# Kernel tuning notes

Hardware: AMD Instinct MI355X
Metric: run time of the kernel (lower is better)

The kernel has to match this reference:

```python
import jax, jax.numpy as jnp
import numpy as np

BITS = 4
GROUP = 128
IN_F = 4096
OUT_F = 11008
N_GROUPS = IN_F // GROUP  # padded_in == in_features here


def fwht(v):
    """Orthonormal fast Walsh-Hadamard transform over the last axis (len = power of 2)."""
    orig = v.shape
    g = orig[-1]
    x = v.reshape(-1, g)
    h = 1
    while h < g:
        x = x.reshape(-1, g // (2 * h), 2, h)
        a, b = x[:, :, 0, :], x[:, :, 1, :]
        x = jnp.stack([a + b, a - b], axis=2).reshape(-1, g)
        h *= 2
    return (x * (1.0 / np.sqrt(g))).reshape(orig)


def setup_inputs() -> dict:
    key = jax.random.key(0)
    ks = jax.random.split(key, 7)
    x = jax.random.normal(ks[0], (4096, IN_F), dtype=jnp.float32)
    # packed 4-bit indices: two per byte, stored as int32 byte values
    packed_weight = jax.random.randint(ks[1], (OUT_F, IN_F // 2), 0, 256, dtype=jnp.int32)
    # per-(row, group) scale factors (positive)
    norms = jax.random.uniform(ks[2], (OUT_F, N_GROUPS), dtype=jnp.float32) * 0.1 + 0.01
    # Lloyd-Max codebook: 2^bits sorted centroids
    centroids = jnp.sort(jax.random.normal(ks[3], (2 ** BITS,), dtype=jnp.float32))
    # Rademacher sign vectors for the two-round signed WHT rotation
    signs1 = jnp.where(jax.random.normal(ks[4], (GROUP,)) >= 0, 1.0, -1.0).astype(jnp.float32)
    signs2 = jnp.where(jax.random.normal(ks[5], (GROUP,)) >= 0, 1.0, -1.0).astype(jnp.float32)
    bias = jax.random.normal(ks[6], (OUT_F,), dtype=jnp.float32) * 0.01
    return {"x": x, "packed_weight": packed_weight, "norms": norms,
            "centroids": centroids, "signs1": signs1, "signs2": signs2, "bias": bias}


def dequantize(packed_weight, norms, centroids, signs1, signs2):
    out_f, n_groups = norms.shape
    # unpack 4-bit nibbles: low nibble at even positions, high nibble at odd
    pw = packed_weight.astype(jnp.uint8)
    lo = (pw & 15).astype(jnp.int32)
    hi = (pw >> 4).astype(jnp.int32)
    idx = jnp.stack([lo, hi], axis=-1).reshape(out_f, -1)      # [out, padded_in]
    c = centroids[idx].reshape(out_f, n_groups, GROUP)          # codebook lookup
    # inverse of rotate(v) = H(s2 * H(s1 * v)):  v = s1 * H(s2 * H(u))
    u = fwht(c) * signs2
    u = fwht(u) * signs1
    w = u * norms[:, :, None]                                   # per-group rescale
    return w.reshape(out_f, -1)


def reference(x, packed_weight, norms, centroids, signs1, signs2, bias):
    w = dequantize(packed_weight, norms, centroids, signs1, signs2)[:, : x.shape[-1]]
    return x @ w.T + bias
```

## Files before the change

kernel.cpp:

```cpp
#include <hip/hip_runtime.h>
#include <stdint.h>

#define M_DIM 4096
#define K_DIM 4096
#define N_DIM 11008
#define N_GROUPS 32

typedef __attribute__((ext_vector_type(8))) short short8;
typedef __attribute__((ext_vector_type(4))) float floatx4;

__device__ __forceinline__ unsigned short f32_to_bf16(float f) {
    unsigned int u = __float_as_uint(f);
    unsigned int rounding = 0x7FFFu + ((u >> 16) & 1u);
    return (unsigned short)((u + rounding) >> 16);
}

__global__ __launch_bounds__(128) void make_M_kernel(
    const float* __restrict__ signs1, const float* __restrict__ signs2,
    unsigned short* __restrict__ Mt)
{
    const int i = blockIdx.x;
    const int j = threadIdx.x;
    __shared__ float s2s[128];
    s2s[j] = signs2[j];
    __syncthreads();
    float acc = 0.f;
#pragma unroll 8
    for (int a = 0; a < 128; ++a) {
        int par = (__popc(i & a) + __popc(a & j)) & 1;
        acc += par ? -s2s[a] : s2s[a];
    }
    Mt[i * 128 + j] = f32_to_bf16(signs1[j] * acc * (1.0f / 128.0f));
}

#define TX_RS 136

__global__ __launch_bounds__(256) void transform_x_kernel(
    const float* __restrict__ x,
    const unsigned short* __restrict__ Mt,
    unsigned short* __restrict__ z)
{
    __shared__ __align__(16) short Xs[64 * TX_RS];
    __shared__ __align__(16) short Ms[128 * TX_RS];

    const int tid = threadIdx.x;
    const int wave = tid >> 6, lane = tid & 63;
    const int col16 = lane & 15, quad = lane >> 4;
    const int m0 = (blockIdx.x >> 5) * 64;
    const int g = blockIdx.x & 31;
    const int c0 = g * 128;

#pragma unroll
    for (int it = 0; it < 8; ++it) {
        int idx = tid + 256 * it;
        int row = idx >> 5, c4 = idx & 31;
        float4 v = *(const float4*)(x + (size_t)(m0 + row) * K_DIM + c0 + c4 * 4);
        uint2 o;
        o.x = (unsigned)f32_to_bf16(v.x) | ((unsigned)f32_to_bf16(v.y) << 16);
        o.y = (unsigned)f32_to_bf16(v.z) | ((unsigned)f32_to_bf16(v.w) << 16);
        *(uint2*)(Xs + row * TX_RS + c4 * 4) = o;
    }
#pragma unroll
    for (int it = 0; it < 8; ++it) {
        int ch = tid + 256 * it;
        int row = ch >> 4, cc = ch & 15;
        uint4 v = *(const uint4*)(Mt + (size_t)ch * 8);
        *(uint4*)(Ms + row * TX_RS + cc * 8) = v;
    }
    __syncthreads();

    floatx4 acc[8] = {};
#pragma unroll
    for (int ks = 0; ks < 4; ++ks) {
        short8 af = *(const short8*)(Xs + (wave * 16 + col16) * TX_RS + ks * 32 + quad * 8);
#pragma unroll
        for (int ni = 0; ni < 8; ++ni) {
            short8 bf = *(const short8*)(Ms + (ni * 16 + col16) * TX_RS + ks * 32 + quad * 8);
            acc[ni] = __builtin_amdgcn_mfma_f32_16x16x32_bf16(af, bf, acc[ni], 0, 0, 0);
        }
    }
#pragma unroll
    for (int ni = 0; ni < 8; ++ni)
#pragma unroll
        for (int r = 0; r < 4; ++r) {
            int row = m0 + wave * 16 + quad * 4 + r;
            z[(size_t)row * K_DIM + c0 + ni * 16 + col16] = f32_to_bf16(acc[ni][r]);
        }
}

__global__ __launch_bounds__(256) void dequant_lut_kernel(
    const int* __restrict__ packed,
    const float* __restrict__ norms,
    const float* __restrict__ centroids,
    unsigned int* __restrict__ w_out)
{
    __shared__ float2 lut[256];
    const int tid = threadIdx.x;
    lut[tid] = make_float2(centroids[tid & 15], centroids[tid >> 4]);
    __syncthreads();

    const int row = blockIdx.x;
    const int g = tid >> 3;
    const float nrm = norms[row * N_GROUPS + g];
    const int* prow = packed + (size_t)row * 2048 + tid * 8;
    int4 pa = *(const int4*)(prow);
    int4 pb = *(const int4*)(prow + 4);
    int v[8] = {pa.x, pa.y, pa.z, pa.w, pb.x, pb.y, pb.z, pb.w};
    unsigned o[8];
#pragma unroll
    for (int q = 0; q < 8; ++q) {
        float2 c = lut[v[q] & 255];
        o[q] = (unsigned)f32_to_bf16(c.x * nrm) | ((unsigned)f32_to_bf16(c.y * nrm) << 16);
    }
    unsigned* orow = w_out + (size_t)row * 2048 + tid * 8;
    *(uint4*)(orow)     = make_uint4(o[0], o[1], o[2], o[3]);
    *(uint4*)(orow + 4) = make_uint4(o[4], o[5], o[6], o[7]);
}

#define BM 256
#define BN 256
#define BK 64

typedef const __attribute__((address_space(1))) void* gvp_t;
typedef __attribute__((address_space(3))) void* svp_t;

#define BARRIER() do { asm volatile("" ::: "memory"); __builtin_amdgcn_s_barrier(); \
                       asm volatile("" ::: "memory"); } while (0)
#define VM8()   asm volatile("s_waitcnt vmcnt(8)" ::: "memory")
#define VM4()   asm volatile("s_waitcnt vmcnt(4)" ::: "memory")
#define VM2()   asm volatile("s_waitcnt vmcnt(2)" ::: "memory")
#define VM0()   asm volatile("s_waitcnt vmcnt(0)" ::: "memory")
#define PRIO1() __builtin_amdgcn_s_setprio(1)
#define PRIO0() __builtin_amdgcn_s_setprio(0)

__device__ __forceinline__ void read_a4(short8 (&dst)[4][2], const short* rb, int s0) {
#pragma unroll
    for (int fm = 0; fm < 4; ++fm) {
        dst[fm][0] = *(const short8*)(rb + fm * 1024 + s0);
        dst[fm][1] = *(const short8*)(rb + fm * 1024 + (s0 ^ 32));
    }
}
__device__ __forceinline__ void read_b2(short8 (&dst)[2][2], const short* rb, int s0) {
#pragma unroll
    for (int fn = 0; fn < 2; ++fn) {
        dst[fn][0] = *(const short8*)(rb + fn * 1024 + s0);
        dst[fn][1] = *(const short8*)(rb + fn * 1024 + (s0 ^ 32));
    }
}
__device__ __forceinline__ void mfma_q(floatx4 (&acc)[4][2],
                                       const short8 (&a)[4][2], const short8 (&b)[2][2]) {
#pragma unroll
    for (int ks = 0; ks < 2; ++ks)
#pragma unroll
        for (int fm = 0; fm < 4; ++fm)
#pragma unroll
            for (int fn = 0; fn < 2; ++fn)
                acc[fm][fn] = __builtin_amdgcn_mfma_f32_16x16x32_bf16(
                    a[fm][ks], b[fn][ks], acc[fm][fn], 0, 0, 0);
}

__global__ __launch_bounds__(512, 2) void gemm_bt_kernel(
    const unsigned short* __restrict__ A,
    const unsigned short* __restrict__ B,
    const float* __restrict__ bias,
    float* __restrict__ C)
{
    __shared__ __align__(16) short smem[65536];
    short* As = smem;
    short* Bs = smem + 32768;

    const int tid = threadIdx.x;
    const int w = tid >> 6, lane = tid & 63;
    const int wm = w >> 2, wn = w & 3;
    const int col16 = lane & 15, quad = lane >> 4;

    const int bid = blockIdx.x;
    const int mt = bid & 15;
    const int nt = bid >> 4;
    const int m0 = mt * BM, n0 = nt * BN;

    const int gc = (lane & 7) ^ (lane >> 3);
    const unsigned short* aSrc = A + (size_t)(m0 + w * 8 + (lane >> 3)) * K_DIM + gc * 8;
    const unsigned short* bSrc = B + (size_t)(n0 + (w >> 2) * 64 + (w & 3) * 8 + (lane >> 3)) * K_DIM + gc * 8;
    const int wOff = w * 512;

#define STAGE_A(BUF, H, KT) do { \
    __builtin_amdgcn_global_load_lds((gvp_t)(aSrc + (size_t)((H) * 64) * K_DIM + (KT) * 64), \
        (svp_t)(As + (BUF) * 16384 + (H) * 8192 + wOff), 16, 0, 0); \
    __builtin_amdgcn_global_load_lds((gvp_t)(aSrc + (size_t)((H) * 64 + 128) * K_DIM + (KT) * 64), \
        (svp_t)(As + (BUF) * 16384 + (H) * 8192 + 4096 + wOff), 16, 0, 0); \
} while (0)
#define STAGE_B(BUF, H, KT) do { \
    __builtin_amdgcn_global_load_lds((gvp_t)(bSrc + (size_t)((H) * 32) * K_DIM + (KT) * 64), \
        (svp_t)(Bs + (BUF) * 16384 + (H) * 8192 + wOff), 16, 0, 0); \
    __builtin_amdgcn_global_load_lds((gvp_t)(bSrc + (size_t)((H) * 32 + 128) * K_DIM + (KT) * 64), \
        (svp_t)(Bs + (BUF) * 16384 + (H) * 8192 + 4096 + wOff), 16, 0, 0); \
} while (0)

    const short* aR = As + (wm * 64 + col16) * 64;
    const short* bR = Bs + (wn * 32 + col16) * 64;
    const int s0 = (quad ^ (col16 & 7)) << 3;

    short8 a0[4][2], a1[4][2], b0[2][2], b1[2][2];
    floatx4 acc[2][2][4][2];
#pragma unroll
    for (int i0 = 0; i0 < 2; ++i0)
#pragma unroll
        for (int i1 = 0; i1 < 2; ++i1)
#pragma unroll
            for (int i2 = 0; i2 < 4; ++i2)
#pragma unroll
                for (int i3 = 0; i3 < 2; ++i3)
                    acc[i0][i1][i2][i3] = (floatx4)0.0f;


    STAGE_A(0, 0, 0); STAGE_B(0, 0, 0);
    STAGE_A(0, 1, 0); STAGE_B(0, 1, 0);
    STAGE_A(1, 0, 1); STAGE_B(1, 0, 1);
    VM8();
    BARRIER();
    read_a4(a0, aR, s0); read_b2(b0, bR, s0);
    STAGE_A(1, 1, 1);
    VM8();
    BARRIER();

    const int NIT = K_DIM / (2 * BK) - 1;
    for (int i = 0; i < NIT; ++i) {
        const int t = 2 * i;
        read_a4(a1, aR + 8192, s0);
        PRIO1(); mfma_q(acc[0][0], a0, b0); PRIO0();
        STAGE_B(1, 1, t + 1);
        VM8(); BARRIER();
        read_b2(b1, bR + 8192, s0);
        PRIO1(); mfma_q(acc[1][0], a1, b0); PRIO0();
        STAGE_A(0, 0, t + 2);
        BARRIER();
        PRIO1(); mfma_q(acc[0][1], a0, b1); PRIO0();
        STAGE_B(0, 0, t + 2);
        VM8(); BARRIER();
        read_a4(a0, aR + 16384, s0); read_b2(b0, bR + 16384, s0);
        PRIO1(); mfma_q(acc[1][1], a1, b1); PRIO0();
        STAGE_A(0, 1, t + 2);
        VM8(); BARRIER();
        read_a4(a1, aR + 16384 + 8192, s0);
        PRIO1(); mfma_q(acc[0][0], a0, b0); PRIO0();
        STAGE_B(0, 1, t + 2);
        VM8(); BARRIER();
        read_b2(b1, bR + 16384 + 8192, s0);
        PRIO1(); mfma_q(acc[1][0], a1, b0); PRIO0();
        STAGE_A(1, 0, t + 3);
        BARRIER();
        PRIO1(); mfma_q(acc[0][1], a0, b1); PRIO0();
        STAGE_B(1, 0, t + 3);
        VM8(); BARRIER();
        read_a4(a0, aR, s0); read_b2(b0, bR, s0);
        PRIO1(); mfma_q(acc[1][1], a1, b1); PRIO0();
        STAGE_A(1, 1, t + 3);
        VM8(); BARRIER();
    }

    read_a4(a1, aR + 8192, s0);
    mfma_q(acc[0][0], a0, b0);
    STAGE_B(1, 1, 63);
    VM8();
    BARRIER();
    read_b2(b1, bR + 8192, s0);
    mfma_q(acc[1][0], a1, b0);
    VM4();
    BARRIER();
    mfma_q(acc[0][1], a0, b1);
    VM2();
    BARRIER();
    read_a4(a0, aR + 16384, s0); read_b2(b0, bR + 16384, s0);
    mfma_q(acc[1][1], a1, b1);
    VM0();
    BARRIER();
    read_a4(a1, aR + 16384 + 8192, s0);
    mfma_q(acc[0][0], a0, b0);
    read_b2(b1, bR + 16384 + 8192, s0);
    mfma_q(acc[1][0], a1, b0);
    mfma_q(acc[0][1], a0, b1);
    mfma_q(acc[1][1], a1, b1);

#undef STAGE_A
#undef STAGE_B

    float bv[2][2];
#pragma unroll
    for (int qn = 0; qn < 2; ++qn)
#pragma unroll
        for (int fn = 0; fn < 2; ++fn)
            bv[qn][fn] = bias[n0 + wn * 64 + qn * 32 + fn * 16 + col16];

#pragma unroll
    for (int qm = 0; qm < 2; ++qm)
#pragma unroll
        for (int fm = 0; fm < 4; ++fm)
#pragma unroll
            for (int r = 0; r < 4; ++r) {
                float* crow = C + (size_t)(m0 + wm * 128 + qm * 64 + fm * 16 + quad * 4 + r) * N_DIM
                              + n0 + wn * 64 + col16;
#pragma unroll
                for (int qn = 0; qn < 2; ++qn)
#pragma unroll
                    for (int fn = 0; fn < 2; ++fn)
                        crow[qn * 32 + fn * 16] = acc[qm][qn][fm][fn][r] + bv[qn][fn];
            }
}

extern "C" void kernel_launch(void* const* d_in, const int* in_sizes, int n_in,
                              void* d_out, int out_size, void* d_ws, size_t ws_size,
                              hipStream_t stream) {
    const float* x        = (const float*)d_in[0];
    const int* packed     = (const int*)d_in[1];
    const float* norms    = (const float*)d_in[2];
    const float* centroids= (const float*)d_in[3];
    const float* signs1   = (const float*)d_in[4];
    const float* signs2   = (const float*)d_in[5];
    const float* bias     = (const float*)d_in[6];
    float* out            = (float*)d_out;

    unsigned short* Mt     = (unsigned short*)d_ws;
    unsigned short* w_bf16 = (unsigned short*)((char*)d_ws + 32768);
    unsigned short* z_bf16 = (unsigned short*)((char*)d_ws + 32768 + (size_t)N_DIM * K_DIM * 2);

    make_M_kernel<<<128, 128, 0, stream>>>(signs1, signs2, Mt);

    transform_x_kernel<<<(M_DIM / 64) * N_GROUPS, 256, 0, stream>>>(x, Mt, z_bf16);

    dequant_lut_kernel<<<N_DIM, 256, 0, stream>>>(
        packed, norms, centroids, (unsigned int*)w_bf16);

    gemm_bt_kernel<<<dim3((M_DIM / BM) * (N_DIM / BN)), 512, 0, stream>>>(
        z_bf16, w_bf16, bias, out);
}
```

Baseline: 593.8 us.

## Restructure x-transform with LDS-staged stores, bank-spread LUT, nontemporal output stores

The x-transform kernel now uses 512-thread blocks that each handle 256 rows in four 64-row steps. Each block keeps its Hadamard-matrix fragments in registers and stages results through LDS so the z writes are coalesced 16-byte stores. The dequant LUT becomes a per-lane replicated 16x32 table to avoid LDS bank conflicts, and the GEMM epilogue writes output with nontemporal stores to reduce cache pollution. The costs are more LDS, extra barriers, and a grid of fewer, larger blocks for the transform.

```diff
diff --git a/kernel.cpp b/kernel.cpp
--- a/kernel.cpp
+++ b/kernel.cpp
@@ -33,59 +33,88 @@
     Mt[i * 128 + j] = f32_to_bf16(signs1[j] * acc * (1.0f / 128.0f));
 }
 
-#define TX_RS 136
-
-__global__ __launch_bounds__(256) void transform_x_kernel(
+__global__ __launch_bounds__(512) void transform_x_kernel(
     const float* __restrict__ x,
     const unsigned short* __restrict__ Mt,
     unsigned short* __restrict__ z)
 {
-    __shared__ __align__(16) short Xs[64 * TX_RS];
-    __shared__ __align__(16) short Ms[128 * TX_RS];
+    __shared__ __align__(16) short Ms[128 * 136];
+    __shared__ __align__(16) short Xs[64 * 136];
+    __shared__ __align__(16) short Ls[64 * 136];
 
     const int tid = threadIdx.x;
     const int wave = tid >> 6, lane = tid & 63;
     const int col16 = lane & 15, quad = lane >> 4;
-    const int m0 = (blockIdx.x >> 5) * 64;
+    const int wr = wave >> 2;
+    const int wc = wave & 3;
     const int g = blockIdx.x & 31;
+    const int mblk = blockIdx.x >> 5;
     const int c0 = g * 128;
-
-#pragma unroll
-    for (int it = 0; it < 8; ++it) {
-        int idx = tid + 256 * it;
-        int row = idx >> 5, c4 = idx & 31;
-        float4 v = *(const float4*)(x + (size_t)(m0 + row) * K_DIM + c0 + c4 * 4);
-        uint2 o;
-        o.x = (unsigned)f32_to_bf16(v.x) | ((unsigned)f32_to_bf16(v.y) << 16);
-        o.y = (unsigned)f32_to_bf16(v.z) | ((unsigned)f32_to_bf16(v.w) << 16);
-        *(uint2*)(Xs + row * TX_RS + c4 * 4) = o;
-    }
-#pragma unroll
-    for (int it = 0; it < 8; ++it) {
-        int ch = tid + 256 * it;
+    const int mBase = mblk * 256;
+
+#pragma unroll
+    for (int it = 0; it < 4; ++it) {
+        int ch = tid + 512 * it;
         int row = ch >> 4, cc = ch & 15;
-        uint4 v = *(const uint4*)(Mt + (size_t)ch * 8);
-        *(uint4*)(Ms + row * TX_RS + cc * 8) = v;
+        *(uint4*)(Ms + row * 136 + cc * 8) = *(const uint4*)(Mt + (size_t)ch * 8);
     }
     __syncthreads();
 
-    floatx4 acc[8] = {};
-#pragma unroll
-    for (int ks = 0; ks < 4; ++ks) {
-        short8 af = *(const short8*)(Xs + (wave * 16 + col16) * TX_RS + ks * 32 + quad * 8);
-#pragma unroll
-        for (int ni = 0; ni < 8; ++ni) {
-            short8 bf = *(const short8*)(Ms + (ni * 16 + col16) * TX_RS + ks * 32 + quad * 8);
-            acc[ni] = __builtin_amdgcn_mfma_f32_16x16x32_bf16(af, bf, acc[ni], 0, 0, 0);
+    short8 bf[2][4];
+#pragma unroll
+    for (int ni = 0; ni < 2; ++ni)
+#pragma unroll
+        for (int ks = 0; ks < 4; ++ks)
+            bf[ni][ks] = *(const short8*)(Ms + (wc * 32 + ni * 16 + col16) * 136 + ks * 32 + quad * 8);
+
+    for (int s = 0; s < 4; ++s) {
+        __syncthreads();
+#pragma unroll
+        for (int it = 0; it < 4; ++it) {
+            int idx = tid + 512 * it;
+            int row = idx >> 5, c4 = idx & 31;
+            float4 v = *(const float4*)(x + (size_t)(mBase + s * 64 + row) * K_DIM + c0 + c4 * 4);
+            uint2 o;
+            o.x = (unsigned)f32_to_bf16(v.x) | ((unsigned)f32_to_bf16(v.y) << 16);
+            o.y = (unsigned)f32_to_bf16(v.z) | ((unsigned)f32_to_bf16(v.w) << 16);
+            *(uint2*)(Xs + row * 136 + c4 * 4) = o;
         }
-    }
-#pragma unroll
-    for (int ni = 0; ni < 8; ++ni)
-#pragma unroll
-        for (int r = 0; r < 4; ++r) {
-            int row = m0 + wave * 16 + quad * 4 + r;
-            z[(size_t)row * K_DIM + c0 + ni * 16 + col16] = f32_to_bf16(acc[ni][r]);
+        __syncthreads();
+
+        short8 af[2][4];
+#pragma unroll
+        for (int mi = 0; mi < 2; ++mi)
+#pragma unroll
+            for (int ks = 0; ks < 4; ++ks)
+                af[mi][ks] = *(const short8*)(Xs + (wr * 32 + mi * 16 + col16) * 136 + ks * 32 + quad * 8);
+        floatx4 acc2[2][2] = {};
+#pragma unroll
+        for (int ks = 0; ks < 4; ++ks)
+#pragma unroll
+            for (int mi = 0; mi < 2; ++mi)
+#pragma unroll
+                for (int ni = 0; ni < 2; ++ni)
+                    acc2[mi][ni] = __builtin_amdgcn_mfma_f32_16x16x32_bf16(
+                        af[mi][ks], bf[ni][ks], acc2[mi][ni], 0, 0, 0);
+
+#pragma unroll
+        for (int mi = 0; mi < 2; ++mi)
+#pragma unroll
+            for (int ni = 0; ni < 2; ++ni)
+#pragma unroll
+                for (int r = 0; r < 4; ++r)
+                    Ls[(wr * 32 + mi * 16 + quad * 4 + r) * 136 + wc * 32 + ni * 16 + col16] =
+                        f32_to_bf16(acc2[mi][ni][r]);
+        __syncthreads();
+
+#pragma unroll
+        for (int it = 0; it < 2; ++it) {
+            int idx = tid + 512 * it;
+            int row = idx >> 4, cc = idx & 15;
+            uint4 v = *(const uint4*)(Ls + row * 136 + cc * 8);
+            *(uint4*)(z + (size_t)(mBase + s * 64 + row) * K_DIM + c0 + cc * 8) = v;
         }
+    }
 }
 
 __global__ __launch_bounds__(256) void dequant_lut_kernel(
@@ -94,10 +123,13 @@
     const float* __restrict__ centroids,
     unsigned int* __restrict__ w_out)
 {
-    __shared__ float2 lut[256];
+    __shared__ float lut[16 * 32];
     const int tid = threadIdx.x;
-    lut[tid] = make_float2(centroids[tid & 15], centroids[tid >> 4]);
+    lut[tid]       = centroids[tid >> 5];
+    lut[tid + 256] = centroids[(tid + 256) >> 5];
     __syncthreads();
+
+    const float* lutr = lut + (tid & 31);
 
     const int row = blockIdx.x;
     const int g = tid >> 3;
@@ -109,8 +141,9 @@
     unsigned o[8];
 #pragma unroll
     for (int q = 0; q < 8; ++q) {
-        float2 c = lut[v[q] & 255];
-        o[q] = (unsigned)f32_to_bf16(c.x * nrm) | ((unsigned)f32_to_bf16(c.y * nrm) << 16);
+        float clo = lutr[(v[q] & 15) << 5];
+        float chi = lutr[((v[q] >> 4) & 15) << 5];
+        o[q] = (unsigned)f32_to_bf16(clo * nrm) | ((unsigned)f32_to_bf16(chi * nrm) << 16);
     }
     unsigned* orow = w_out + (size_t)row * 2048 + tid * 8;
     *(uint4*)(orow)     = make_uint4(o[0], o[1], o[2], o[3]);
@@ -304,7 +337,8 @@
                 for (int qn = 0; qn < 2; ++qn)
 #pragma unroll
                     for (int fn = 0; fn < 2; ++fn)
-                        crow[qn * 32 + fn * 16] = acc[qm][qn][fm][fn][r] + bv[qn][fn];
+                        __builtin_nontemporal_store(acc[qm][qn][fm][fn][r] + bv[qn][fn],
+                                                    &crow[qn * 32 + fn * 16]);
             }
 }
 
@@ -326,7 +360,7 @@
 
     make_M_kernel<<<128, 128, 0, stream>>>(signs1, signs2, Mt);
 
-    transform_x_kernel<<<(M_DIM / 64) * N_GROUPS, 256, 0, stream>>>(x, Mt, z_bf16);
+    transform_x_kernel<<<(M_DIM / 256) * N_GROUPS, 512, 0, stream>>>(x, Mt, z_bf16);
 
     dequant_lut_kernel<<<N_DIM, 256, 0, stream>>>(
         packed, norms, centroids, (unsigned int*)w_bf16);
```

New measurement: 589.0 us. Within noise of the previous version (-0.8%).
